# Optimization experiments

Hardware: AMD Instinct MI355X
Metric: run time of the kernel (lower is better)

Reference implementation:

```python
import jax, jax.numpy as jnp
import numpy as np

BS = 32  # leaf block size


def setup_inputs() -> dict:
    key = jax.random.key(0)
    ks = jax.random.split(key, 10)
    N, C, E, H = 262144, 128, 4194304, 4
    x = jax.random.normal(ks[0], (1, N, C), jnp.float32)
    rows = jax.random.randint(ks[1], (E,), 0, N, dtype=jnp.int32)
    offs = jax.random.randint(ks[2], (E,), -16, 16, dtype=jnp.int32)
    cols = jnp.clip(rows + offs, 0, N - 1)
    edge_index = jnp.stack([rows, cols], axis=0)  # (2, E) int32
    edge_values = jax.random.normal(ks[3], (E,), jnp.float32)
    positions = jax.random.uniform(ks[4], (N, 3), jnp.float32)
    qkv_w = jax.random.normal(ks[5], (C, 3 * C), jnp.float32) * 0.02
    qkv_b = jnp.zeros((3 * C,), jnp.float32)
    proj_w = jax.random.normal(ks[6], (C, C), jnp.float32) * 0.02
    proj_b = jnp.zeros((C,), jnp.float32)
    gate_w = jax.random.normal(ks[7], (H, 1), jnp.float32) * 0.01  # nn.Linear(1, H)
    gate_b = jnp.zeros((H,), jnp.float32)
    return {"x": x, "edge_index": edge_index, "edge_values": edge_values,
            "positions": positions, "qkv_w": qkv_w, "qkv_b": qkv_b,
            "proj_w": proj_w, "proj_b": proj_b, "gate_w": gate_w, "gate_b": gate_b}


def _build_leaf_block_connectivity(edge_index, edge_values, positions, num_blocks, dtype):
    # Returns attn_mask (nb, 32, 33) and edge_feats (nb, 32, 33, 4) = (dx,dy,dz,w).
    rows, cols = edge_index[0], edge_index[1]
    br, bc = rows // BS, cols // BS
    in_blk = (br == bc) & (br < num_blocks)
    b_safe = jnp.where(in_blk, br, num_blocks)  # out-of-block edges -> dummy block
    rl, cl = rows % BS, cols % BS
    dx = positions[cols] - positions[rows]               # (E, 3)
    ef_flat = jnp.concatenate([dx, edge_values[:, None]], axis=1).astype(dtype)  # (E, 4)
    diag = jnp.arange(BS)
    attn_mask = jnp.zeros((num_blocks + 1, BS, BS + 1), dtype)
    attn_mask = attn_mask.at[:, diag, diag].set(1.0)      # self
    attn_mask = attn_mask.at[:, :, BS].set(1.0)           # block node
    attn_mask = attn_mask.at[b_safe, rl, cl].set(1.0)     # edges
    edge_feats = jnp.zeros((num_blocks + 1, BS, BS + 1, 4), dtype)
    edge_feats = edge_feats.at[b_safe, rl, cl].set(ef_flat)
    return attn_mask[:num_blocks], edge_feats[:num_blocks]


def reference(x, edge_index, edge_values, positions, qkv_w, qkv_b, proj_w, proj_b, gate_w, gate_b):
    B, N, C = x.shape
    H = gate_b.shape[0]
    hd = C // H
    scale = hd ** -0.5
    nb = N // BS
    dtype = x.dtype
    attn_mask, edge_feats = _build_leaf_block_connectivity(edge_index, edge_values, positions, nb, dtype)

    x_blk = x.reshape(B, nb, BS, C)
    block_node = x_blk.mean(axis=2, keepdims=True)            # (B, nb, 1, C)
    kv = jnp.concatenate([x_blk, block_node], axis=2)          # (B, nb, 33, C)
    qkv_q = x_blk @ qkv_w + qkv_b
    qkv_kv = kv @ qkv_w + qkv_b
    q = qkv_q[..., :C].reshape(B, nb, BS, H, hd)
    k = qkv_kv[..., C:2 * C].reshape(B, nb, BS + 1, H, hd)
    v = qkv_kv[..., 2 * C:].reshape(B, nb, BS + 1, H, hd)

    scores = jnp.einsum('bnqhd,bnkhd->bnqkh', q, k) * scale    # (B, nb, 32, 33, H)

    diag = jnp.arange(BS)
    w_bias = edge_feats[..., 3]                                # (nb, 32, 33)
    w_bias = w_bias.at[:, :, BS].set(1.0)
    w_bias = w_bias.at[:, diag, diag].set(1.0)
    scores = scores + w_bias[None, :, :, :, None]

    mask = attn_mask[None, :, :, :, None]                      # (1, nb, 32, 33, 1)
    neg = jnp.asarray(-1e9, dtype)
    scores = jnp.where(mask == 0, neg, scores)
    attn_probs = jax.nn.softmax(scores, axis=3)

    # edge_gate: Linear(1, H) applied to w_bias, zeroed where masked, added post-softmax
    gate = w_bias[..., None] * gate_w[:, 0] + gate_b           # (nb, 32, 33, H)
    gate = jnp.where(mask[0] == 0, 0.0, gate)[None]            # (1, nb, 32, 33, H)
    combined = attn_probs + gate

    out = jnp.einsum('bnqkh,bnkhd->bnqhd', combined, v).reshape(B, N, C)
    return out @ proj_w + proj_b
```

## Files before the change

kernel.cpp:

```cpp
#include <hip/hip_runtime.h>
#include <hip/hip_bf16.h>

#define BS 32
#define NBC 33

typedef unsigned long long ull;
typedef __attribute__((ext_vector_type(8))) __bf16 bf16x8;
typedef __attribute__((ext_vector_type(4))) float f32x4;
typedef __attribute__((ext_vector_type(4))) unsigned short us4;

__device__ __forceinline__ unsigned short f2b(float f) {
    __hip_bfloat16 h = __float2bfloat16(f);
    return *reinterpret_cast<unsigned short*>(&h);
}
__device__ __forceinline__ float b2f(unsigned short u) {
    union { unsigned int i; float f; } x; x.i = ((unsigned int)u) << 16; return x.f;
}
#define LD8(p) (*reinterpret_cast<const bf16x8*>(p))

#define ZB 2048
__global__ void zero_prepack_kernel(uint4* __restrict__ tbl4, int n4,
                                    const float* __restrict__ qkv_w,
                                    const float* __restrict__ proj_w,
                                    unsigned short* __restrict__ wq,
                                    unsigned short* __restrict__ wp) {
    if (blockIdx.x < ZB) {
        int stride = ZB * 256;
        for (int i = blockIdx.x * 256 + threadIdx.x; i < n4; i += stride)
            tbl4[i] = make_uint4(0u, 0u, 0u, 0u);
    } else {
        int tid = (blockIdx.x - ZB) * 256 + threadIdx.x;
        int f = tid >> 9, lane = (tid >> 3) & 63, j = tid & 7;
        int ks = f & 3;
        int kk = ks * 32 + (lane >> 4) * 8 + j;
        int nn = lane & 15;
        if (f < 96) {
            int t = f >> 2;
            int w = t / 6, s = t % 6;
            int g = (s < 2) ? (2 * w + s) : (s < 4) ? (8 + 2 * w + (s - 2)) : (16 + 2 * w + (s - 4));
            wq[tid] = f2b(qkv_w[kk * 384 + g * 16 + nn]);
        } else {
            int f2 = f - 96;
            wp[f2 * 512 + lane * 8 + j] = f2b(proj_w[kk * 128 + (f2 >> 2) * 16 + nn]);
        }
    }
}

__global__ void edge_scatter_kernel(const int* __restrict__ rows,
                                    const int* __restrict__ cols,
                                    const float* __restrict__ vals,
                                    ull* __restrict__ tbl, int E) {
    int base = (blockIdx.x * 256 + threadIdx.x) * 4;
    if (base >= E) return;
    if (base + 4 <= E) {
        int4 r4 = *reinterpret_cast<const int4*>(rows + base);
        int4 c4 = *reinterpret_cast<const int4*>(cols + base);
        float4 v4 = *reinterpret_cast<const float4*>(vals + base);
        int rr[4] = {r4.x, r4.y, r4.z, r4.w};
        int cc[4] = {c4.x, c4.y, c4.z, c4.w};
        float vv[4] = {v4.x, v4.y, v4.z, v4.w};
        #pragma unroll
        for (int k = 0; k < 4; ++k) {
            int r = rr[k], c = cc[k];
            if ((r >> 5) == (c >> 5) && r != c) {
                ull key = ((ull)(unsigned)(base + k + 1) << 32) | (ull)__float_as_uint(vv[k]);
                atomicMax(&tbl[((size_t)(r >> 5) * BS + (r & 31)) * NBC + (c & 31)], key);
            }
        }
    } else {
        for (int e = base; e < E && e < base + 4; ++e) {
            int r = rows[e], c = cols[e];
            if ((r >> 5) == (c >> 5) && r != c) {
                ull key = ((ull)(unsigned)(e + 1) << 32) | (ull)__float_as_uint(vals[e]);
                atomicMax(&tbl[((size_t)(r >> 5) * BS + (r & 31)) * NBC + (c & 31)], key);
            }
        }
    }
}

__global__ __launch_bounds__(256)
void block_attn_kernel(const float* __restrict__ x,
                       const ull* __restrict__ tbl,
                       const unsigned short* __restrict__ wq,
                       const unsigned short* __restrict__ wp,
                       const float* __restrict__ qkv_b,
                       const float* __restrict__ proj_b,
                       const float* __restrict__ gate_w,
                       const float* __restrict__ gate_b,
                       float* __restrict__ out) {
    __shared__ __align__(16) unsigned char smem[31872];
    unsigned short (*qs)[32][40]  = (unsigned short (*)[32][40])(smem);
    unsigned short (*ksm)[34][40] = (unsigned short (*)[34][40])(smem + 10240);
    unsigned short (*vT)[32][40]  = (unsigned short (*)[32][40])(smem + 21120);
    float (*pcol)[32]             = (float (*)[32])(smem + 31360);
    unsigned short (*xs)[136]     = (unsigned short (*)[136])(smem + 21120);

    const int b = blockIdx.x, t = threadIdx.x;
    const int w = t >> 6, l = t & 63, g16 = l >> 4, c16 = l & 15;
    const f32x4 z4 = {0.f, 0.f, 0.f, 0.f};
    const float NEG = -1.0e30f;

    const float* xb = x + (size_t)b * (BS * 128);
    #pragma unroll
    for (int it = 0; it < 4; ++it) {
        int idx = (t + it * 256) * 4;
        float4 v = *reinterpret_cast<const float4*>(xb + idx);
        us4 u; u.x = f2b(v.x); u.y = f2b(v.y); u.z = f2b(v.z); u.w = f2b(v.w);
        *reinterpret_cast<us4*>(&xs[idx >> 7][idx & 127]) = u;
    }
    if (l < 32) ksm[w][33][l] = 0;

    float wb[2][4][3];
    {
        const ull* tb = tbl + (size_t)b * (BS * NBC);
        #pragma unroll
        for (int mt = 0; mt < 2; ++mt)
            #pragma unroll
            for (int r = 0; r < 4; ++r) {
                const int i = 16 * mt + 4 * g16 + r;
                #pragma unroll
                for (int nt = 0; nt < 2; ++nt) {
                    const int j = 16 * nt + c16;
                    const ull wv = tb[i * NBC + j];
                    wb[mt][r][nt] = (j == i) ? 1.f
                                   : (wv ? __uint_as_float((unsigned)(wv & 0xffffffffu)) : NEG);
                }
                wb[mt][r][2] = (c16 == 0) ? 1.f : NEG;
            }
    }
    __syncthreads();

    bf16x8 a[2][4];
    #pragma unroll
    for (int mt = 0; mt < 2; ++mt)
        #pragma unroll
        for (int ks = 0; ks < 4; ++ks)
            a[mt][ks] = LD8(&xs[c16 + 16 * mt][ks * 32 + g16 * 8]);
    __syncthreads();

    {
        const unsigned short* wqs = wq + (size_t)(w * 24) * 512 + l * 8;
        #pragma unroll
        for (int s = 0; s < 6; ++s) {
            bf16x8 bn[4];
            #pragma unroll
            for (int ks = 0; ks < 4; ++ks) bn[ks] = LD8(wqs + (s * 4 + ks) * 512);
            f32x4 acc0 = z4, acc1 = z4;
            #pragma unroll
            for (int ks = 0; ks < 4; ++ks) {
                acc0 = __builtin_amdgcn_mfma_f32_16x16x32_bf16(a[0][ks], bn[ks], acc0, 0, 0, 0);
                acc1 = __builtin_amdgcn_mfma_f32_16x16x32_bf16(a[1][ks], bn[ks], acc1, 0, 0, 0);
            }
            const float bias = qkv_b[(s >> 1) * 128 + 32 * w + 16 * (s & 1) + c16];
            const int cc = 16 * (s & 1) + c16;
            if (s < 2) {
                #pragma unroll
                for (int r = 0; r < 4; ++r) {
                    qs[w][4 * g16 + r][cc]      = f2b(acc0[r] + bias);
                    qs[w][16 + 4 * g16 + r][cc] = f2b(acc1[r] + bias);
                }
            } else {
                float csum = acc0[0] + acc0[1] + acc0[2] + acc0[3]
                           + acc1[0] + acc1[1] + acc1[2] + acc1[3];
                csum += __shfl_xor(csum, 16, 64);
                csum += __shfl_xor(csum, 32, 64);
                const float meanv = csum * (1.f / 32.f) + bias;
                if (s < 4) {
                    #pragma unroll
                    for (int r = 0; r < 4; ++r) {
                        ksm[w][4 * g16 + r][cc]      = f2b(acc0[r] + bias);
                        ksm[w][16 + 4 * g16 + r][cc] = f2b(acc1[r] + bias);
                    }
                    if (g16 == 0) ksm[w][32][cc] = f2b(meanv);
                } else {
                    #pragma unroll
                    for (int r = 0; r < 4; ++r) {
                        vT[w][cc][4 * g16 + r]      = f2b(acc0[r] + bias);
                        vT[w][cc][16 + 4 * g16 + r] = f2b(acc1[r] + bias);
                    }
                    if (g16 == 0) vT[w][cc][32] = f2b(meanv);
                }
            }
        }
    }
    __syncthreads();

    f32x4 s[2][3];
    {
        bf16x8 aq0 = LD8(&qs[w][c16][g16 * 8]);
        bf16x8 aq1 = LD8(&qs[w][16 + c16][g16 * 8]);
        bf16x8 bk0 = LD8(&ksm[w][c16][g16 * 8]);
        bf16x8 bk1 = LD8(&ksm[w][16 + c16][g16 * 8]);
        const int n2 = (c16 == 0) ? 32 : 33;
        bf16x8 bk2 = LD8(&ksm[w][n2][g16 * 8]);
        s[0][0] = __builtin_amdgcn_mfma_f32_16x16x32_bf16(aq0, bk0, z4, 0, 0, 0);
        s[0][1] = __builtin_amdgcn_mfma_f32_16x16x32_bf16(aq0, bk1, z4, 0, 0, 0);
        s[0][2] = __builtin_amdgcn_mfma_f32_16x16x32_bf16(aq0, bk2, z4, 0, 0, 0);
        s[1][0] = __builtin_amdgcn_mfma_f32_16x16x32_bf16(aq1, bk0, z4, 0, 0, 0);
        s[1][1] = __builtin_amdgcn_mfma_f32_16x16x32_bf16(aq1, bk1, z4, 0, 0, 0);
        s[1][2] = __builtin_amdgcn_mfma_f32_16x16x32_bf16(aq1, bk2, z4, 0, 0, 0);
    }

    {
        const float scale = 0.17677669529663687f;
        const float gwh = gate_w[w], gbh = gate_b[w];
        #pragma unroll
        for (int mt = 0; mt < 2; ++mt)
            #pragma unroll
            for (int r = 0; r < 4; ++r) {
                const int i = 16 * mt + 4 * g16 + r;
                float sc[3];
                #pragma unroll
                for (int k = 0; k < 3; ++k) sc[k] = s[mt][k][r] * scale + wb[mt][r][k];
                float mx = fmaxf(fmaxf(sc[0], sc[1]), sc[2]);
                mx = fmaxf(mx, __shfl_xor(mx, 1, 64));
                mx = fmaxf(mx, __shfl_xor(mx, 2, 64));
                mx = fmaxf(mx, __shfl_xor(mx, 4, 64));
                mx = fmaxf(mx, __shfl_xor(mx, 8, 64));
                float e0 = __expf(sc[0] - mx), e1 = __expf(sc[1] - mx), e2 = __expf(sc[2] - mx);
                float sum = e0 + e1 + e2;
                sum += __shfl_xor(sum, 1, 64);
                sum += __shfl_xor(sum, 2, 64);
                sum += __shfl_xor(sum, 4, 64);
                sum += __shfl_xor(sum, 8, 64);
                const float inv = __builtin_amdgcn_rcpf(sum);
                float gt0 = (wb[mt][r][0] > -1.0e29f) ? wb[mt][r][0] * gwh + gbh : 0.f;
                float gt1 = (wb[mt][r][1] > -1.0e29f) ? wb[mt][r][1] * gwh + gbh : 0.f;
                float gt2 = (wb[mt][r][2] > -1.0e29f) ? gwh + gbh : 0.f;
                qs[w][i][c16]      = f2b(e0 * inv + gt0);
                qs[w][i][16 + c16] = f2b(e1 * inv + gt1);
                if (c16 == 0) pcol[w][i] = e2 * inv + gt2;
            }
    }
    __syncthreads();

    {
        bf16x8 ap0 = LD8(&qs[w][c16][g16 * 8]);
        bf16x8 ap1 = LD8(&qs[w][16 + c16][g16 * 8]);
        f32x4 o[2][2];
        #pragma unroll
        for (int nt = 0; nt < 2; ++nt) {
            bf16x8 bv = LD8(&vT[w][16 * nt + c16][g16 * 8]);
            o[0][nt] = __builtin_amdgcn_mfma_f32_16x16x32_bf16(ap0, bv, z4, 0, 0, 0);
            o[1][nt] = __builtin_amdgcn_mfma_f32_16x16x32_bf16(ap1, bv, z4, 0, 0, 0);
        }
        #pragma unroll
        for (int nt = 0; nt < 2; ++nt) {
            const float vm = b2f(vT[w][16 * nt + c16][32]);
            #pragma unroll
            for (int mt = 0; mt < 2; ++mt)
                #pragma unroll
                for (int r = 0; r < 4; ++r)
                    o[mt][nt][r] += pcol[w][16 * mt + 4 * g16 + r] * vm;
        }
        #pragma unroll
        for (int mt = 0; mt < 2; ++mt)
            #pragma unroll
            for (int nt = 0; nt < 2; ++nt)
                #pragma unroll
                for (int r = 0; r < 4; ++r)
                    qs[w][16 * mt + 4 * g16 + r][16 * nt + c16] = f2b(o[mt][nt][r]);
    }
    __syncthreads();

    {
        bf16x8 aa[2][4];
        #pragma unroll
        for (int mt = 0; mt < 2; ++mt)
            #pragma unroll
            for (int h = 0; h < 4; ++h)
                aa[mt][h] = LD8(&qs[h][c16 + 16 * mt][g16 * 8]);
        f32x4 po[2][2];
        po[0][0] = z4; po[0][1] = z4; po[1][0] = z4; po[1][1] = z4;
        const unsigned short* wps = wp + l * 8;
        #pragma unroll
        for (int nt = 0; nt < 2; ++nt)
            #pragma unroll
            for (int h = 0; h < 4; ++h) {
                bf16x8 bw = LD8(wps + (size_t)((2 * w + nt) * 4 + h) * 512);
                po[0][nt] = __builtin_amdgcn_mfma_f32_16x16x32_bf16(aa[0][h], bw, po[0][nt], 0, 0, 0);
                po[1][nt] = __builtin_amdgcn_mfma_f32_16x16x32_bf16(aa[1][h], bw, po[1][nt], 0, 0, 0);
            }
        float* ob = out + (size_t)b * (BS * 128);
        #pragma unroll
        for (int nt = 0; nt < 2; ++nt) {
            const int col = 32 * w + 16 * nt + c16;
            const float pbv = proj_b[col];
            #pragma unroll
            for (int mt = 0; mt < 2; ++mt)
                #pragma unroll
                for (int r = 0; r < 4; ++r)
                    ob[(size_t)(16 * mt + 4 * g16 + r) * 128 + col] = po[mt][nt][r] + pbv;
        }
    }
}

extern "C" void kernel_launch(void* const* d_in, const int* in_sizes, int n_in,
                              void* d_out, int out_size, void* d_ws, size_t ws_size,
                              hipStream_t stream) {
    const float* x      = (const float*)d_in[0];
    const int*   ei     = (const int*)d_in[1];
    const float* ev     = (const float*)d_in[2];
    const float* qkv_w  = (const float*)d_in[4];
    const float* qkv_b  = (const float*)d_in[5];
    const float* proj_w = (const float*)d_in[6];
    const float* proj_b = (const float*)d_in[7];
    const float* gate_w = (const float*)d_in[8];
    const float* gate_b = (const float*)d_in[9];
    float* out = (float*)d_out;

    const int E  = in_sizes[2];
    const int N  = in_sizes[0] / 128;
    const int nb = N / BS;

    ull* tbl = (ull*)d_ws;
    size_t twords = (size_t)nb * BS * NBC;
    size_t tbytes = (twords * sizeof(ull) + 255) & ~(size_t)255;
    unsigned short* wqp = (unsigned short*)((char*)d_ws + tbytes);
    unsigned short* wpp = wqp + 96 * 512;

    zero_prepack_kernel<<<ZB + 256, 256, 0, stream>>>((uint4*)tbl,
                                                      (int)(twords * sizeof(ull) / 16),
                                                      qkv_w, proj_w, wqp, wpp);
    edge_scatter_kernel<<<((E + 3) / 4 + 255) / 256, 256, 0, stream>>>(ei, ei + E, ev, tbl, E);
    block_attn_kernel<<<nb, 256, 0, stream>>>(x, tbl, wqp, wpp, qkv_b, proj_b,
                                              gate_w, gate_b, out);
}
```

Before: 259.1 us.

## Shrink LDS footprint, prefetch QKV weights, and raise MFMA wave priority

Cuts shared memory per block by dropping the padded zero K row and the float pcol array. The post-softmax block-node column is now stored as bf16 in a spare column of vT, and the zero K operand is built in registers instead. Adds launch bounds with a minimum of 5 blocks per CU, software-prefetches the next QKV weight slice during the current MFMAs, and wraps MFMA groups in s_setprio. The aim is higher occupancy and better latency hiding. The cost is register pressure from the prefetch buffers under a tighter register cap, which may cause spills, and slightly lower precision for the block-node probability.

```diff
diff --git a/kernel.cpp b/kernel.cpp
--- a/kernel.cpp
+++ b/kernel.cpp
@@ -78,7 +78,7 @@
     }
 }
 
-__global__ __launch_bounds__(256)
+__global__ __launch_bounds__(256, 5)
 void block_attn_kernel(const float* __restrict__ x,
                        const ull* __restrict__ tbl,
                        const unsigned short* __restrict__ wq,
@@ -88,12 +88,11 @@
                        const float* __restrict__ gate_w,
                        const float* __restrict__ gate_b,
                        float* __restrict__ out) {
-    __shared__ __align__(16) unsigned char smem[31872];
+    __shared__ __align__(16) unsigned char smem[31040];
     unsigned short (*qs)[32][40]  = (unsigned short (*)[32][40])(smem);
-    unsigned short (*ksm)[34][40] = (unsigned short (*)[34][40])(smem + 10240);
-    unsigned short (*vT)[32][40]  = (unsigned short (*)[32][40])(smem + 21120);
-    float (*pcol)[32]             = (float (*)[32])(smem + 31360);
-    unsigned short (*xs)[136]     = (unsigned short (*)[136])(smem + 21120);
+    unsigned short (*ksm)[33][40] = (unsigned short (*)[33][40])(smem + 10240);
+    unsigned short (*vT)[32][40]  = (unsigned short (*)[32][40])(smem + 20800);
+    unsigned short (*xs)[136]     = (unsigned short (*)[136])(smem + 20800);
 
     const int b = blockIdx.x, t = threadIdx.x;
     const int w = t >> 6, l = t & 63, g16 = l >> 4, c16 = l & 15;
@@ -108,7 +107,6 @@
         us4 u; u.x = f2b(v.x); u.y = f2b(v.y); u.z = f2b(v.z); u.w = f2b(v.w);
         *reinterpret_cast<us4*>(&xs[idx >> 7][idx & 127]) = u;
     }
-    if (l < 32) ksm[w][33][l] = 0;
 
     float wb[2][4][3];
     {
@@ -140,17 +138,26 @@
 
     {
         const unsigned short* wqs = wq + (size_t)(w * 24) * 512 + l * 8;
+        bf16x8 bn[4];
+        #pragma unroll
+        for (int ks = 0; ks < 4; ++ks) bn[ks] = LD8(wqs + ks * 512);
         #pragma unroll
         for (int s = 0; s < 6; ++s) {
-            bf16x8 bn[4];
-            #pragma unroll
-            for (int ks = 0; ks < 4; ++ks) bn[ks] = LD8(wqs + (s * 4 + ks) * 512);
+            bf16x8 bc[4];
+            #pragma unroll
+            for (int ks = 0; ks < 4; ++ks) bc[ks] = bn[ks];
+            if (s < 5) {
+                #pragma unroll
+                for (int ks = 0; ks < 4; ++ks) bn[ks] = LD8(wqs + ((s + 1) * 4 + ks) * 512);
+            }
             f32x4 acc0 = z4, acc1 = z4;
+            __builtin_amdgcn_s_setprio(1);
             #pragma unroll
             for (int ks = 0; ks < 4; ++ks) {
-                acc0 = __builtin_amdgcn_mfma_f32_16x16x32_bf16(a[0][ks], bn[ks], acc0, 0, 0, 0);
-                acc1 = __builtin_amdgcn_mfma_f32_16x16x32_bf16(a[1][ks], bn[ks], acc1, 0, 0, 0);
-            }
+                acc0 = __builtin_amdgcn_mfma_f32_16x16x32_bf16(a[0][ks], bc[ks], acc0, 0, 0, 0);
+                acc1 = __builtin_amdgcn_mfma_f32_16x16x32_bf16(a[1][ks], bc[ks], acc1, 0, 0, 0);
+            }
+            __builtin_amdgcn_s_setprio(0);
             const float bias = qkv_b[(s >> 1) * 128 + 32 * w + 16 * (s & 1) + c16];
             const int cc = 16 * (s & 1) + c16;
             if (s < 2) {
@@ -191,14 +198,19 @@
         bf16x8 aq1 = LD8(&qs[w][16 + c16][g16 * 8]);
         bf16x8 bk0 = LD8(&ksm[w][c16][g16 * 8]);
         bf16x8 bk1 = LD8(&ksm[w][16 + c16][g16 * 8]);
-        const int n2 = (c16 == 0) ? 32 : 33;
-        bf16x8 bk2 = LD8(&ksm[w][n2][g16 * 8]);
+        bf16x8 bk2 = LD8(&ksm[w][32][g16 * 8]);
+        bf16x8 zb;
+        #pragma unroll
+        for (int q = 0; q < 8; ++q) zb[q] = (__bf16)0.f;
+        if (c16 != 0) bk2 = zb;
+        __builtin_amdgcn_s_setprio(1);
         s[0][0] = __builtin_amdgcn_mfma_f32_16x16x32_bf16(aq0, bk0, z4, 0, 0, 0);
         s[0][1] = __builtin_amdgcn_mfma_f32_16x16x32_bf16(aq0, bk1, z4, 0, 0, 0);
         s[0][2] = __builtin_amdgcn_mfma_f32_16x16x32_bf16(aq0, bk2, z4, 0, 0, 0);
         s[1][0] = __builtin_amdgcn_mfma_f32_16x16x32_bf16(aq1, bk0, z4, 0, 0, 0);
         s[1][1] = __builtin_amdgcn_mfma_f32_16x16x32_bf16(aq1, bk1, z4, 0, 0, 0);
         s[1][2] = __builtin_amdgcn_mfma_f32_16x16x32_bf16(aq1, bk2, z4, 0, 0, 0);
+        __builtin_amdgcn_s_setprio(0);
     }
 
     {
@@ -229,7 +241,7 @@
                 float gt2 = (wb[mt][r][2] > -1.0e29f) ? gwh + gbh : 0.f;
                 qs[w][i][c16]      = f2b(e0 * inv + gt0);
                 qs[w][i][16 + c16] = f2b(e1 * inv + gt1);
-                if (c16 == 0) pcol[w][i] = e2 * inv + gt2;
+                if (c16 == 0) vT[w][i][33] = f2b(e2 * inv + gt2);
             }
     }
     __syncthreads();
@@ -238,12 +250,14 @@
         bf16x8 ap0 = LD8(&qs[w][c16][g16 * 8]);
         bf16x8 ap1 = LD8(&qs[w][16 + c16][g16 * 8]);
         f32x4 o[2][2];
+        __builtin_amdgcn_s_setprio(1);
         #pragma unroll
         for (int nt = 0; nt < 2; ++nt) {
             bf16x8 bv = LD8(&vT[w][16 * nt + c16][g16 * 8]);
             o[0][nt] = __builtin_amdgcn_mfma_f32_16x16x32_bf16(ap0, bv, z4, 0, 0, 0);
             o[1][nt] = __builtin_amdgcn_mfma_f32_16x16x32_bf16(ap1, bv, z4, 0, 0, 0);
         }
+        __builtin_amdgcn_s_setprio(0);
         #pragma unroll
         for (int nt = 0; nt < 2; ++nt) {
             const float vm = b2f(vT[w][16 * nt + c16][32]);
@@ -251,7 +265,7 @@
             for (int mt = 0; mt < 2; ++mt)
                 #pragma unroll
                 for (int r = 0; r < 4; ++r)
-                    o[mt][nt][r] += pcol[w][16 * mt + 4 * g16 + r] * vm;
+                    o[mt][nt][r] += b2f(vT[w][16 * mt + 4 * g16 + r][33]) * vm;
         }
         #pragma unroll
         for (int mt = 0; mt < 2; ++mt)
@@ -274,13 +288,22 @@
         po[0][0] = z4; po[0][1] = z4; po[1][0] = z4; po[1][1] = z4;
         const unsigned short* wps = wp + l * 8;
         #pragma unroll
-        for (int nt = 0; nt < 2; ++nt)
-            #pragma unroll
-            for (int h = 0; h < 4; ++h) {
-                bf16x8 bw = LD8(wps + (size_t)((2 * w + nt) * 4 + h) * 512);
-                po[0][nt] = __builtin_amdgcn_mfma_f32_16x16x32_bf16(aa[0][h], bw, po[0][nt], 0, 0, 0);
-                po[1][nt] = __builtin_amdgcn_mfma_f32_16x16x32_bf16(aa[1][h], bw, po[1][nt], 0, 0, 0);
-            }
+        for (int nt = 0; nt < 2; ++nt) {
+            bf16x8 bw0 = LD8(wps + (size_t)((2 * w + nt) * 4 + 0) * 512);
+            bf16x8 bw1 = LD8(wps + (size_t)((2 * w + nt) * 4 + 1) * 512);
+            bf16x8 bw2 = LD8(wps + (size_t)((2 * w + nt) * 4 + 2) * 512);
+            bf16x8 bw3 = LD8(wps + (size_t)((2 * w + nt) * 4 + 3) * 512);
+            __builtin_amdgcn_s_setprio(1);
+            po[0][nt] = __builtin_amdgcn_mfma_f32_16x16x32_bf16(aa[0][0], bw0, po[0][nt], 0, 0, 0);
+            po[1][nt] = __builtin_amdgcn_mfma_f32_16x16x32_bf16(aa[1][0], bw0, po[1][nt], 0, 0, 0);
+            po[0][nt] = __builtin_amdgcn_mfma_f32_16x16x32_bf16(aa[0][1], bw1, po[0][nt], 0, 0, 0);
+            po[1][nt] = __builtin_amdgcn_mfma_f32_16x16x32_bf16(aa[1][1], bw1, po[1][nt], 0, 0, 0);
+            po[0][nt] = __builtin_amdgcn_mfma_f32_16x16x32_bf16(aa[0][2], bw2, po[0][nt], 0, 0, 0);
+            po[1][nt] = __builtin_amdgcn_mfma_f32_16x16x32_bf16(aa[1][2], bw2, po[1][nt], 0, 0, 0);
+            po[0][nt] = __builtin_amdgcn_mfma_f32_16x16x32_bf16(aa[0][3], bw3, po[0][nt], 0, 0, 0);
+            po[1][nt] = __builtin_amdgcn_mfma_f32_16x16x32_bf16(aa[1][3], bw3, po[1][nt], 0, 0, 0);
+            __builtin_amdgcn_s_setprio(0);
+        }
         float* ob = out + (size_t)b * (BS * 128);
         #pragma unroll
         for (int nt = 0; nt < 2; ++nt) {
```

Result: slower. 308.6 us (+19.1%).
